# Kernel tuning notes

Measured on AMD Instinct MI355X. Metric: run time of the kernel, lower is better.

Reference implementation:

```python
import jax, jax.numpy as jnp
import numpy as np

N = 100_000   # nodes in batched graph
E = 1_000_000 # edges
B = 1024      # graphs in batch
H = 64        # hidden_dim


def setup_inputs() -> dict:
    key = jax.random.key(0)
    ks = jax.random.split(key, 12)
    u_flag = jax.random.randint(ks[0], (N,), 0, 2) > 0
    v_flag = jax.random.randint(ks[1], (N,), 0, 2) > 0
    src = jax.random.randint(ks[2], (E,), 0, N, dtype=jnp.int32)
    dst = jax.random.randint(ks[3], (E,), 0, N, dtype=jnp.int32)
    # contiguous graph assignment so every graph is non-empty
    node2graph = ((jnp.arange(N, dtype=jnp.int32) * B) // N).astype(jnp.int32)
    s = 0.05
    params = {
        'W0': jax.random.normal(ks[4], (2, H), jnp.float32) * s,
        'b0': jnp.zeros((H,), jnp.float32),
        'eps0': jnp.zeros((), jnp.float32),
        'W1': jax.random.normal(ks[5], (H, H), jnp.float32) * s,
        'b1': jnp.zeros((H,), jnp.float32),
        'eps1': jnp.zeros((), jnp.float32),
        'W2': jax.random.normal(ks[6], (H, H), jnp.float32) * s,
        'b2': jnp.zeros((H,), jnp.float32),
        'eps2': jnp.zeros((), jnp.float32),
        'Ws1': jax.random.normal(ks[7], (H, H), jnp.float32) * s,
        'bs1': jnp.zeros((H,), jnp.float32),
        'Ws2': jax.random.normal(ks[8], (H, 1), jnp.float32) * s,
        'bs2': jnp.zeros((1,), jnp.float32),
    }
    return dict(u_flag=u_flag, v_flag=v_flag, src=src, dst=dst,
                node2graph=node2graph, **params)


def _gin_layer(h, src, dst, W, b, eps):
    # GINConv: MLP((1+eps)*h + sum_{j->i} h_j), apply_func = Linear
    agg = jax.ops.segment_sum(h[src], dst, num_segments=N)  # [N,H_in]
    z = (1.0 + eps) * h + agg
    return jax.nn.relu(z @ W + b)


def reference(u_flag, v_flag, src, dst, node2graph,
              W0, b0, eps0, W1, b1, eps1, W2, b2, eps2,
              Ws1, bs1, Ws2, bs2):
    # one-hot node features from u/v masks: feat[:,0]=u, feat[:,1]=v
    feat = jnp.stack([u_flag, v_flag], axis=-1).astype(jnp.float32)  # [N,2]
    h = _gin_layer(feat, src, dst, W0, b0, eps0)
    h = _gin_layer(h, src, dst, W1, b1, eps1)
    h = _gin_layer(h, src, dst, W2, b2, eps2)  # [N,H]
    # per-graph mean pooling (dgl.mean_nodes)
    sums = jax.ops.segment_sum(h, node2graph, num_segments=B)          # [B,H]
    cnts = jax.ops.segment_sum(jnp.ones((N,), jnp.float32), node2graph,
                               num_segments=B)                         # [B]
    hg = sums / jnp.maximum(cnts, 1.0)[:, None]
    # Scorer: Linear -> ReLU -> Linear -> sigmoid
    z = jax.nn.relu(hg @ Ws1 + bs1)
    return jax.nn.sigmoid(z @ Ws2 + bs2)[:, 0]  # (B,)
```

## Files before the change

### kernel.cpp

```cpp
#include <hip/hip_runtime.h>
#include <hip/hip_bf16.h>
#include <math.h>

#define NN 100000
#define NE 1000000
#define NB 1024
#define NCHUNK 6250
#define NRNG 256
#define RANGE 391
#define NBK 512
#define EPB 1954

typedef __attribute__((ext_vector_type(8))) short short8v;
typedef __attribute__((ext_vector_type(4))) float f32x4;

union frag16 { uint4 u; short8v s; };

static __device__ __forceinline__ float bf_lo(unsigned int u) {
    return __uint_as_float(u << 16);
}
static __device__ __forceinline__ float bf_hi(unsigned int u) {
    return __uint_as_float(u & 0xffff0000u);
}
static __device__ __forceinline__ unsigned int bf16_rne(float f) {
    unsigned int u = __float_as_uint(f);
    return (u + 0x7fffu + ((u >> 16) & 1u)) >> 16;
}
static __device__ __forceinline__ unsigned int pack_bf16(float a, float b) {
    return bf16_rne(a) | (bf16_rne(b) << 16);
}

__global__ __launch_bounds__(256) void featb_kernel(
        const void* __restrict__ u, const void* __restrict__ v,
        unsigned char* __restrict__ featb,
        const int* __restrict__ n2g, int* __restrict__ gstart, int n) {
    __shared__ int flag_s;
    const int tid = threadIdx.x;
    int c = 0;
    {
        const unsigned char* p = (const unsigned char*)u + tid * 4;
        c = (p[0] != 0) + (p[1] != 0) + (p[2] != 0) + (p[3] != 0);
    }
    #pragma unroll
    for (int off = 32; off > 0; off >>= 1) c += __shfl_xor(c, off);
    if (tid == 0) flag_s = 0;
    __syncthreads();
    if ((tid & 63) == 0) atomicAdd(&flag_s, c);
    __syncthreads();
    bool is_u8 = (4 * flag_s > 1024);
    int i = blockIdx.x * blockDim.x + tid;
    if (i >= n) return;
    unsigned char fu, fv;
    if (is_u8) {
        fu = ((const unsigned char*)u)[i] ? 1 : 0;
        fv = ((const unsigned char*)v)[i] ? 1 : 0;
    } else {
        fu = ((const int*)u)[i] ? 1 : 0;
        fv = ((const int*)v)[i] ? 1 : 0;
    }
    featb[i] = fu | (fv << 1);
    int g = n2g[i];
    if (i == 0) {
        gstart[g] = 0;
        gstart[NB] = n;
    } else if (n2g[i - 1] != g) {
        gstart[g] = i;
    }
}

__global__ __launch_bounds__(256) void bcount_kernel(const int* __restrict__ dst,
                                                     int* __restrict__ bcnt, int e) {
    __shared__ int hc[NRNG];
    hc[threadIdx.x] = 0;
    __syncthreads();
    const int blk = blockIdx.x, lo = blk * EPB, hi = min(e, lo + EPB);
    for (int i = lo + threadIdx.x; i < hi; i += 256)
        atomicAdd(&hc[dst[i] / RANGE], 1);
    __syncthreads();
    bcnt[threadIdx.x * NBK + blk] = hc[threadIdx.x];
}

__global__ __launch_bounds__(256) void bsum_kernel(const int* __restrict__ bcnt,
                                                   int* __restrict__ btot) {
    __shared__ int s[4];
    const int b = blockIdx.x, tid = threadIdx.x;
    int c = bcnt[b * NBK + tid] + bcnt[b * NBK + 256 + tid];
    #pragma unroll
    for (int off = 32; off > 0; off >>= 1) c += __shfl_xor(c, off);
    if ((tid & 63) == 0) s[tid >> 6] = c;
    __syncthreads();
    if (tid == 0) btot[b] = s[0] + s[1] + s[2] + s[3];
}

__global__ __launch_bounds__(256) void bbase_kernel(const int* __restrict__ bcnt,
                                                    const int* __restrict__ btot,
                                                    int* __restrict__ bstart,
                                                    int* __restrict__ bbase) {
    __shared__ int s[256];
    const int b = blockIdx.x, tid = threadIdx.x;
    int v = btot[tid];
    s[tid] = v;
    __syncthreads();
    for (int off = 1; off < 256; off <<= 1) {
        int t = (tid >= off) ? s[tid - off] : 0;
        __syncthreads();
        s[tid] += t;
        __syncthreads();
    }
    if (b == 0) {
        bstart[tid] = s[tid] - v;
        if (tid == 255) bstart[NRNG] = s[tid];
    }
    const int exb = s[b] - btot[b];
    __syncthreads();
    int2 c = ((const int2*)(bcnt + b * NBK))[tid];
    int lsum = c.x + c.y;
    s[tid] = lsum;
    __syncthreads();
    for (int off = 1; off < 256; off <<= 1) {
        int t = (tid >= off) ? s[tid - off] : 0;
        __syncthreads();
        s[tid] += t;
        __syncthreads();
    }
    int run = exb + s[tid] - lsum;
    ((int2*)(bbase + b * NBK))[tid] = make_int2(run, run + c.x);
}

__global__ __launch_bounds__(256) void bwrite_kernel(const int* __restrict__ src,
                                                     const int* __restrict__ dst,
                                                     const int* __restrict__ bbase,
                                                     unsigned int* __restrict__ ebuck, int e) {
    __shared__ int cur[NRNG];
    const int blk = blockIdx.x;
    cur[threadIdx.x] = bbase[threadIdx.x * NBK + blk];
    __syncthreads();
    const int lo = blk * EPB, hi = min(e, lo + EPB);
    for (int i = lo + threadIdx.x; i < hi; i += 256) {
        int d = dst[i];
        int b = d / RANGE;
        int dloc = d - b * RANGE;
        int pos = atomicAdd(&cur[b], 1);
        ebuck[pos] = (unsigned int)src[i] | ((unsigned int)dloc << 17);
    }
}

__global__ __launch_bounds__(256) void build_kernel(
        const unsigned int* __restrict__ ebuck, const int* __restrict__ bstart,
        const unsigned char* __restrict__ featb,
        const float* __restrict__ W0, const float* __restrict__ b0,
        const float* __restrict__ epsp,
        int* __restrict__ rowptr, int* __restrict__ esrc,
        unsigned short* __restrict__ hout) {
    __shared__ unsigned long long hloc[RANGE];
    __shared__ int cur[RANGE];
    __shared__ int sscan[256];
    __shared__ float w0s[128];
    __shared__ float b0s[64];
    const int r = blockIdx.x, tid = threadIdx.x;
    const int nlo = r * RANGE;
    const int nr = min(NN, nlo + RANGE) - nlo;
    for (int i = tid; i < nr; i += 256) hloc[i] = 0ull;
    if (tid < 128) w0s[tid] = W0[tid];
    if (tid >= 128 && tid < 192) b0s[tid - 128] = b0[tid - 128];
    __syncthreads();
    const int elo = bstart[r], ehi = bstart[r + 1];
    for (int i = elo + tid; i < ehi; i += 256) {
        unsigned int u = ebuck[i];
        unsigned char f = featb[u & 0x1FFFFu];
        unsigned long long inc = 1ull
            | ((unsigned long long)(f & 1) << 21)
            | ((unsigned long long)(f >> 1) << 42);
        atomicAdd(&hloc[u >> 17], inc);
    }
    __syncthreads();
    const int base = tid * 2;
    int ldeg[2];
    int lsum = 0;
    #pragma unroll
    for (int j = 0; j < 2; ++j) {
        int i = base + j;
        ldeg[j] = (i < nr) ? (int)(hloc[i] & 0x1FFFFFull) : 0;
        lsum += ldeg[j];
    }
    sscan[tid] = lsum;
    __syncthreads();
    for (int off = 1; off < 256; off <<= 1) {
        int t = (tid >= off) ? sscan[tid - off] : 0;
        __syncthreads();
        sscan[tid] += t;
        __syncthreads();
    }
    int run = elo + sscan[tid] - lsum;
    #pragma unroll
    for (int j = 0; j < 2; ++j) {
        int i = base + j;
        if (i < nr) {
            rowptr[nlo + i] = run;
            cur[i] = run;
            run += ldeg[j];
        }
    }
    if (r == NRNG - 1 && tid == 0) rowptr[NN] = bstart[NRNG];
    __syncthreads();
    for (int i = elo + tid; i < ehi; i += 256) {
        unsigned int u = ebuck[i];
        int pos = atomicAdd(&cur[u >> 17], 1);
        esrc[pos] = (int)(u & 0x1FFFFu);
    }
    const float e = 1.0f + epsp[0];
    for (int idx = tid; idx < nr * 8; idx += 256) {
        int i = idx >> 3, oct = idx & 7;
        unsigned long long hv = hloc[i];
        float cu = (float)((hv >> 21) & 0x1FFFFFull);
        float cv = (float)(hv >> 42);
        unsigned char f = featb[nlo + i];
        float z0 = fmaf(e, (float)(f & 1), cu);
        float z1 = fmaf(e, (float)(f >> 1), cv);
        unsigned int p[4];
        #pragma unroll
        for (int k = 0; k < 4; ++k) {
            int c0 = oct * 8 + 2 * k;
            float o0 = fmaxf(fmaf(z0, w0s[c0],     fmaf(z1, w0s[64 + c0],     b0s[c0])),     0.0f);
            float o1 = fmaxf(fmaf(z0, w0s[c0 + 1], fmaf(z1, w0s[64 + c0 + 1], b0s[c0 + 1])), 0.0f);
            p[k] = pack_bf16(o0, o1);
        }
        ((uint4*)(hout + (size_t)(nlo + i) * 64))[oct] = make_uint4(p[0], p[1], p[2], p[3]);
    }
}

__global__ __launch_bounds__(64) void wprep_kernel(const float* __restrict__ W1,
                                                   const float* __restrict__ W2,
                                                   uint4* __restrict__ wpk1,
                                                   uint4* __restrict__ wpk2) {
    const float* W = blockIdx.x ? W2 : W1;
    uint4* wpk = blockIdx.x ? wpk2 : wpk1;
    const int lane = threadIdx.x;
    const int bcol = lane & 15;
    const int krow = (lane >> 4) * 8;
    #pragma unroll
    for (int n = 0; n < 4; ++n) {
        #pragma unroll
        for (int t = 0; t < 2; ++t) {
            unsigned int p[4];
            #pragma unroll
            for (int jj = 0; jj < 4; ++jj) {
                int k0 = t * 32 + krow + 2 * jj;
                float w0 = W[(size_t)k0 * 64 + n * 16 + bcol];
                float w1 = W[(size_t)(k0 + 1) * 64 + n * 16 + bcol];
                p[jj] = pack_bf16(w0, w1);
            }
            wpk[(n * 2 + t) * 64 + lane] = make_uint4(p[0], p[1], p[2], p[3]);
        }
    }
}

__global__ __launch_bounds__(256) void gin_layer_kernel(
        const int* __restrict__ rowptr, const int* __restrict__ esrc,
        const unsigned short* __restrict__ hin,
        const uint4* __restrict__ wpk, const float* __restrict__ b,
        const float* __restrict__ epsp, unsigned short* __restrict__ hout) {
    __shared__ __align__(16) unsigned char zall[4][2048];
    const int tid = threadIdx.x;
    const int lane = tid & 63;
    const int g = lane >> 3;
    const int sub = lane & 7;
    unsigned char* zw = &zall[tid >> 6][0];
    const float ep = 1.0f + epsp[0];

    const int bcol = (lane & 15);
    frag16 Bf[4][2];
    #pragma unroll
    for (int n = 0; n < 4; ++n) {
        #pragma unroll
        for (int t = 0; t < 2; ++t)
            Bf[n][t].u = wpk[(n * 2 + t) * 64 + lane];
    }
    float bj[4];
    #pragma unroll
    for (int n = 0; n < 4; ++n) bj[n] = b[n * 16 + bcol];

    const int wid = (blockIdx.x * blockDim.x + tid) >> 6;
    const int nwaves = (gridDim.x * blockDim.x) >> 6;

    for (int chunk = wid; chunk < NCHUNK; chunk += nwaves) {
        const int cbase_n = chunk * 16;
        #pragma unroll
        for (int b8 = 0; b8 < 2; ++b8) {
            int node = cbase_n + b8 * 8 + g;
            int e0 = rowptr[node], e1 = rowptr[node + 1];
            int deg = e1 - e0;
            uint4 ov = ((const uint4*)(hin + (size_t)node * 64))[sub];
            float acc[8];
            #pragma unroll
            for (int c = 0; c < 8; ++c) acc[c] = 0.0f;
            int md = deg;
            md = max(md, __shfl_xor(md, 8));
            md = max(md, __shfl_xor(md, 16));
            md = max(md, __shfl_xor(md, 32));
            #pragma unroll 4
            for (int t = 0; t < md; ++t) {
                int em = max(min(e0 + t, e1 - 1), 0);
                int sraw = esrc[em];
                bool act = (t < deg);
                int s = act ? sraw : node;
                uint4 v = ((const uint4*)(hin + (size_t)s * 64))[sub];
                float m = act ? 1.0f : 0.0f;
                acc[0] = fmaf(m, bf_lo(v.x), acc[0]);
                acc[1] = fmaf(m, bf_hi(v.x), acc[1]);
                acc[2] = fmaf(m, bf_lo(v.y), acc[2]);
                acc[3] = fmaf(m, bf_hi(v.y), acc[3]);
                acc[4] = fmaf(m, bf_lo(v.z), acc[4]);
                acc[5] = fmaf(m, bf_hi(v.z), acc[5]);
                acc[6] = fmaf(m, bf_lo(v.w), acc[6]);
                acc[7] = fmaf(m, bf_hi(v.w), acc[7]);
            }
            acc[0] = fmaf(ep, bf_lo(ov.x), acc[0]);
            acc[1] = fmaf(ep, bf_hi(ov.x), acc[1]);
            acc[2] = fmaf(ep, bf_lo(ov.y), acc[2]);
            acc[3] = fmaf(ep, bf_hi(ov.y), acc[3]);
            acc[4] = fmaf(ep, bf_lo(ov.z), acc[4]);
            acc[5] = fmaf(ep, bf_hi(ov.z), acc[5]);
            acc[6] = fmaf(ep, bf_lo(ov.w), acc[6]);
            acc[7] = fmaf(ep, bf_hi(ov.w), acc[7]);
            uint4 pk = make_uint4(pack_bf16(acc[0], acc[1]), pack_bf16(acc[2], acc[3]),
                                  pack_bf16(acc[4], acc[5]), pack_bf16(acc[6], acc[7]));
            int row = b8 * 8 + g;
            *(uint4*)&zw[row * 128 + ((sub ^ g) << 4)] = pk;
        }
        const int arow = lane & 15;
        const int hi = lane >> 4;
        frag16 a0, a1;
        a0.u = *(const uint4*)&zw[arow * 128 + (((hi + 0) ^ (lane & 7)) << 4)];
        a1.u = *(const uint4*)&zw[arow * 128 + (((hi + 4) ^ (lane & 7)) << 4)];
        #pragma unroll
        for (int n = 0; n < 4; ++n) {
            f32x4 c = {bj[n], bj[n], bj[n], bj[n]};
            c = __builtin_amdgcn_mfma_f32_16x16x32_bf16(a0.s, Bf[n][0].s, c, 0, 0, 0);
            c = __builtin_amdgcn_mfma_f32_16x16x32_bf16(a1.s, Bf[n][1].s, c, 0, 0, 0);
            #pragma unroll
            for (int q = 0; q < 4; ++q) {
                int rr = hi * 4 + q;
                float v = fmaxf(c[q], 0.0f);
                hout[(size_t)(cbase_n + rr) * 64 + n * 16 + bcol] =
                    (unsigned short)bf16_rne(v);
            }
        }
    }
}

__global__ __launch_bounds__(256) void pool_scorer_kernel(
        const unsigned short* __restrict__ h, const int* __restrict__ gstart,
        const float* __restrict__ Ws1, const float* __restrict__ bs1,
        const float* __restrict__ Ws2, const float* __restrict__ bs2,
        float* __restrict__ out) {
    int g = blockIdx.x * 4 + (threadIdx.x >> 6);
    int lane = threadIdx.x & 63;
    if (g >= NB) return;
    int s0 = gstart[g], s1 = gstart[g + 1];
    float a0 = 0.0f, a1 = 0.0f, a2 = 0.0f, a3 = 0.0f;
    int i = s0;
    for (; i + 4 <= s1; i += 4) {
        a0 += __uint_as_float((unsigned int)h[(size_t)(i    ) * 64 + lane] << 16);
        a1 += __uint_as_float((unsigned int)h[(size_t)(i + 1) * 64 + lane] << 16);
        a2 += __uint_as_float((unsigned int)h[(size_t)(i + 2) * 64 + lane] << 16);
        a3 += __uint_as_float((unsigned int)h[(size_t)(i + 3) * 64 + lane] << 16);
    }
    for (; i < s1; ++i)
        a0 += __uint_as_float((unsigned int)h[(size_t)i * 64 + lane] << 16);
    float mean = ((a0 + a1) + (a2 + a3)) / fmaxf((float)(s1 - s0), 1.0f);
    float o = bs1[lane];
    #pragma unroll 8
    for (int k = 0; k < 64; ++k)
        o = fmaf(__shfl(mean, k), Ws1[(size_t)k * 64 + lane], o);
    float z = fmaxf(o, 0.0f) * Ws2[lane];
    #pragma unroll
    for (int off = 32; off > 0; off >>= 1) z += __shfl_xor(z, off);
    if (lane == 0) out[g] = 1.0f / (1.0f + expf(-(z + bs2[0])));
}

extern "C" void kernel_launch(void* const* d_in, const int* in_sizes, int n_in,
                              void* d_out, int out_size, void* d_ws, size_t ws_size,
                              hipStream_t stream) {
    const void*  u_flag = d_in[0];
    const void*  v_flag = d_in[1];
    const int*   src    = (const int*)d_in[2];
    const int*   dst    = (const int*)d_in[3];
    const int*   n2g    = (const int*)d_in[4];
    const float* W0     = (const float*)d_in[5];
    const float* b0     = (const float*)d_in[6];
    const float* eps0   = (const float*)d_in[7];
    const float* W1     = (const float*)d_in[8];
    const float* b1     = (const float*)d_in[9];
    const float* eps1   = (const float*)d_in[10];
    const float* W2     = (const float*)d_in[11];
    const float* b2     = (const float*)d_in[12];
    const float* eps2   = (const float*)d_in[13];
    const float* Ws1    = (const float*)d_in[14];
    const float* bs1    = (const float*)d_in[15];
    const float* Ws2    = (const float*)d_in[16];
    const float* bs2    = (const float*)d_in[17];
    float* out = (float*)d_out;

    int*    ws     = (int*)d_ws;
    int*    rowptr = ws;
    int*    gstart = ws + 100008;
    unsigned char* featb = (unsigned char*)(ws + 101036);
    unsigned short* h_a = (unsigned short*)(ws + 126036);
    unsigned short* h_b = (unsigned short*)(ws + 3326036);
    int*    esrc   = ws + 6526036;
    int*    bcnt   = ws + 7526036;
    int*    bbase  = ws + 7657108;
    int*    bstart = ws + 7788180;
    int*    btot   = ws + 7788440;
    unsigned int* ebuck = (unsigned int*)(ws + 7788696);
    uint4*  wpk1   = (uint4*)(ws + 8788696);
    uint4*  wpk2   = (uint4*)(ws + 8790744);

    const int B256 = 256;

    featb_kernel<<<(NN + B256 - 1) / B256, B256, 0, stream>>>(u_flag, v_flag, featb,
                                                              n2g, gstart, NN);

    wprep_kernel<<<2, 64, 0, stream>>>(W1, W2, wpk1, wpk2);

    bcount_kernel<<<NBK, B256, 0, stream>>>(dst, bcnt, NE);
    bsum_kernel<<<NRNG, B256, 0, stream>>>(bcnt, btot);
    bbase_kernel<<<NRNG, B256, 0, stream>>>(bcnt, btot, bstart, bbase);
    bwrite_kernel<<<NBK, B256, 0, stream>>>(src, dst, bbase, ebuck, NE);

    build_kernel<<<NRNG, B256, 0, stream>>>(ebuck, bstart, featb, W0, b0, eps0,
                                            rowptr, esrc, h_a);

    gin_layer_kernel<<<1563, 256, 0, stream>>>(rowptr, esrc, h_a, wpk1, b1, eps1, h_b);
    gin_layer_kernel<<<1563, 256, 0, stream>>>(rowptr, esrc, h_b, wpk2, b2, eps2, h_a);

    pool_scorer_kernel<<<NB / 4, 256, 0, stream>>>(h_a, gstart, Ws1, bs1, Ws2, bs2, out);
}
```

Measured before the change: 137.6 us.

## Merge prep kernels into fewer launches and batch edge-index loads via shuffles

The featb and bcount kernels are merged into one launch using a block-index split, and the bsum and wprep kernels are merged the same way, which removes two kernel launches and their gaps. In the GIN aggregation loop, each 8-lane group now loads eight source indices at once, one per lane, and broadcasts them with shuffles. Before, every lane loaded the same index on every iteration. This cuts redundant index loads and the serial dependency on them, at the cost of extra shuffle instructions.

```diff
diff --git a/kernel.cpp b/kernel.cpp
--- a/kernel.cpp
+++ b/kernel.cpp
@@ -10,6 +10,7 @@
 #define RANGE 391
 #define NBK 512
 #define EPB 1954
+#define FEATB_BLKS 392
 
 typedef __attribute__((ext_vector_type(8))) short short8v;
 typedef __attribute__((ext_vector_type(4))) float f32x4;
@@ -30,66 +31,93 @@
     return bf16_rne(a) | (bf16_rne(b) << 16);
 }
 
-__global__ __launch_bounds__(256) void featb_kernel(
+__global__ __launch_bounds__(256) void prep_kernel(
         const void* __restrict__ u, const void* __restrict__ v,
         unsigned char* __restrict__ featb,
-        const int* __restrict__ n2g, int* __restrict__ gstart, int n) {
-    __shared__ int flag_s;
+        const int* __restrict__ n2g, int* __restrict__ gstart,
+        const int* __restrict__ dst, int* __restrict__ bcnt) {
+    __shared__ int sh[NRNG];
     const int tid = threadIdx.x;
-    int c = 0;
-    {
-        const unsigned char* p = (const unsigned char*)u + tid * 4;
-        c = (p[0] != 0) + (p[1] != 0) + (p[2] != 0) + (p[3] != 0);
-    }
-    #pragma unroll
-    for (int off = 32; off > 0; off >>= 1) c += __shfl_xor(c, off);
-    if (tid == 0) flag_s = 0;
-    __syncthreads();
-    if ((tid & 63) == 0) atomicAdd(&flag_s, c);
-    __syncthreads();
-    bool is_u8 = (4 * flag_s > 1024);
-    int i = blockIdx.x * blockDim.x + tid;
-    if (i >= n) return;
-    unsigned char fu, fv;
-    if (is_u8) {
-        fu = ((const unsigned char*)u)[i] ? 1 : 0;
-        fv = ((const unsigned char*)v)[i] ? 1 : 0;
+    if (blockIdx.x < FEATB_BLKS) {
+        int c;
+        {
+            const unsigned char* p = (const unsigned char*)u + tid * 4;
+            c = (p[0] != 0) + (p[1] != 0) + (p[2] != 0) + (p[3] != 0);
+        }
+        #pragma unroll
+        for (int off = 32; off > 0; off >>= 1) c += __shfl_xor(c, off);
+        if (tid == 0) sh[0] = 0;
+        __syncthreads();
+        if ((tid & 63) == 0) atomicAdd(&sh[0], c);
+        __syncthreads();
+        bool is_u8 = (4 * sh[0] > 1024);
+        int i = blockIdx.x * 256 + tid;
+        if (i >= NN) return;
+        unsigned char fu, fv;
+        if (is_u8) {
+            fu = ((const unsigned char*)u)[i] ? 1 : 0;
+            fv = ((const unsigned char*)v)[i] ? 1 : 0;
+        } else {
+            fu = ((const int*)u)[i] ? 1 : 0;
+            fv = ((const int*)v)[i] ? 1 : 0;
+        }
+        featb[i] = fu | (fv << 1);
+        int g = n2g[i];
+        if (i == 0) {
+            gstart[g] = 0;
+            gstart[NB] = NN;
+        } else if (n2g[i - 1] != g) {
+            gstart[g] = i;
+        }
     } else {
-        fu = ((const int*)u)[i] ? 1 : 0;
-        fv = ((const int*)v)[i] ? 1 : 0;
-    }
-    featb[i] = fu | (fv << 1);
-    int g = n2g[i];
-    if (i == 0) {
-        gstart[g] = 0;
-        gstart[NB] = n;
-    } else if (n2g[i - 1] != g) {
-        gstart[g] = i;
-    }
-}
-
-__global__ __launch_bounds__(256) void bcount_kernel(const int* __restrict__ dst,
-                                                     int* __restrict__ bcnt, int e) {
-    __shared__ int hc[NRNG];
-    hc[threadIdx.x] = 0;
-    __syncthreads();
-    const int blk = blockIdx.x, lo = blk * EPB, hi = min(e, lo + EPB);
-    for (int i = lo + threadIdx.x; i < hi; i += 256)
-        atomicAdd(&hc[dst[i] / RANGE], 1);
-    __syncthreads();
-    bcnt[threadIdx.x * NBK + blk] = hc[threadIdx.x];
-}
-
-__global__ __launch_bounds__(256) void bsum_kernel(const int* __restrict__ bcnt,
-                                                   int* __restrict__ btot) {
+        const int blk = blockIdx.x - FEATB_BLKS;
+        sh[tid] = 0;
+        __syncthreads();
+        const int lo = blk * EPB, hi = min(NE, lo + EPB);
+        for (int i = lo + tid; i < hi; i += 256)
+            atomicAdd(&sh[dst[i] / RANGE], 1);
+        __syncthreads();
+        bcnt[tid * NBK + blk] = sh[tid];
+    }
+}
+
+__global__ __launch_bounds__(256) void wsum_kernel(
+        const int* __restrict__ bcnt, int* __restrict__ btot,
+        const float* __restrict__ W1, const float* __restrict__ W2,
+        uint4* __restrict__ wpk1, uint4* __restrict__ wpk2) {
     __shared__ int s[4];
-    const int b = blockIdx.x, tid = threadIdx.x;
-    int c = bcnt[b * NBK + tid] + bcnt[b * NBK + 256 + tid];
-    #pragma unroll
-    for (int off = 32; off > 0; off >>= 1) c += __shfl_xor(c, off);
-    if ((tid & 63) == 0) s[tid >> 6] = c;
-    __syncthreads();
-    if (tid == 0) btot[b] = s[0] + s[1] + s[2] + s[3];
+    const int tid = threadIdx.x;
+    if (blockIdx.x < NRNG) {
+        const int b = blockIdx.x;
+        int c = bcnt[b * NBK + tid] + bcnt[b * NBK + 256 + tid];
+        #pragma unroll
+        for (int off = 32; off > 0; off >>= 1) c += __shfl_xor(c, off);
+        if ((tid & 63) == 0) s[tid >> 6] = c;
+        __syncthreads();
+        if (tid == 0) btot[b] = s[0] + s[1] + s[2] + s[3];
+    } else {
+        if (tid >= 64) return;
+        const float* W = (blockIdx.x == NRNG) ? W1 : W2;
+        uint4* wpk = (blockIdx.x == NRNG) ? wpk1 : wpk2;
+        const int lane = tid;
+        const int bcol = lane & 15;
+        const int krow = (lane >> 4) * 8;
+        #pragma unroll
+        for (int n = 0; n < 4; ++n) {
+            #pragma unroll
+            for (int t = 0; t < 2; ++t) {
+                unsigned int p[4];
+                #pragma unroll
+                for (int jj = 0; jj < 4; ++jj) {
+                    int k0 = t * 32 + krow + 2 * jj;
+                    float w0 = W[(size_t)k0 * 64 + n * 16 + bcol];
+                    float w1 = W[(size_t)(k0 + 1) * 64 + n * 16 + bcol];
+                    p[jj] = pack_bf16(w0, w1);
+                }
+                wpk[(n * 2 + t) * 64 + lane] = make_uint4(p[0], p[1], p[2], p[3]);
+            }
+        }
+    }
 }
 
 __global__ __launch_bounds__(256) void bbase_kernel(const int* __restrict__ bcnt,
@@ -229,32 +257,6 @@
     }
 }
 
-__global__ __launch_bounds__(64) void wprep_kernel(const float* __restrict__ W1,
-                                                   const float* __restrict__ W2,
-                                                   uint4* __restrict__ wpk1,
-                                                   uint4* __restrict__ wpk2) {
-    const float* W = blockIdx.x ? W2 : W1;
-    uint4* wpk = blockIdx.x ? wpk2 : wpk1;
-    const int lane = threadIdx.x;
-    const int bcol = lane & 15;
-    const int krow = (lane >> 4) * 8;
-    #pragma unroll
-    for (int n = 0; n < 4; ++n) {
-        #pragma unroll
-        for (int t = 0; t < 2; ++t) {
-            unsigned int p[4];
-            #pragma unroll
-            for (int jj = 0; jj < 4; ++jj) {
-                int k0 = t * 32 + krow + 2 * jj;
-                float w0 = W[(size_t)k0 * 64 + n * 16 + bcol];
-                float w1 = W[(size_t)(k0 + 1) * 64 + n * 16 + bcol];
-                p[jj] = pack_bf16(w0, w1);
-            }
-            wpk[(n * 2 + t) * 64 + lane] = make_uint4(p[0], p[1], p[2], p[3]);
-        }
-    }
-}
-
 __global__ __launch_bounds__(256) void gin_layer_kernel(
         const int* __restrict__ rowptr, const int* __restrict__ esrc,
         const unsigned short* __restrict__ hin,
@@ -298,22 +300,26 @@
             md = max(md, __shfl_xor(md, 8));
             md = max(md, __shfl_xor(md, 16));
             md = max(md, __shfl_xor(md, 32));
-            #pragma unroll 4
-            for (int t = 0; t < md; ++t) {
-                int em = max(min(e0 + t, e1 - 1), 0);
-                int sraw = esrc[em];
-                bool act = (t < deg);
-                int s = act ? sraw : node;
-                uint4 v = ((const uint4*)(hin + (size_t)s * 64))[sub];
-                float m = act ? 1.0f : 0.0f;
-                acc[0] = fmaf(m, bf_lo(v.x), acc[0]);
-                acc[1] = fmaf(m, bf_hi(v.x), acc[1]);
-                acc[2] = fmaf(m, bf_lo(v.y), acc[2]);
-                acc[3] = fmaf(m, bf_hi(v.y), acc[3]);
-                acc[4] = fmaf(m, bf_lo(v.z), acc[4]);
-                acc[5] = fmaf(m, bf_hi(v.z), acc[5]);
-                acc[6] = fmaf(m, bf_lo(v.w), acc[6]);
-                acc[7] = fmaf(m, bf_hi(v.w), acc[7]);
+            for (int tb = 0; tb < md; tb += 8) {
+                int ei = max(min(e0 + tb + sub, e1 - 1), 0);
+                int sidx = esrc[ei];
+                #pragma unroll 4
+                for (int tt = 0; tt < 8; ++tt) {
+                    int t = tb + tt;
+                    int s_ = __shfl(sidx, (lane & 56) + tt);
+                    bool act = (t < deg);
+                    int s = act ? s_ : node;
+                    uint4 v = ((const uint4*)(hin + (size_t)s * 64))[sub];
+                    float m = act ? 1.0f : 0.0f;
+                    acc[0] = fmaf(m, bf_lo(v.x), acc[0]);
+                    acc[1] = fmaf(m, bf_hi(v.x), acc[1]);
+                    acc[2] = fmaf(m, bf_lo(v.y), acc[2]);
+                    acc[3] = fmaf(m, bf_hi(v.y), acc[3]);
+                    acc[4] = fmaf(m, bf_lo(v.z), acc[4]);
+                    acc[5] = fmaf(m, bf_hi(v.z), acc[5]);
+                    acc[6] = fmaf(m, bf_lo(v.w), acc[6]);
+                    acc[7] = fmaf(m, bf_hi(v.w), acc[7]);
+                }
             }
             acc[0] = fmaf(ep, bf_lo(ov.x), acc[0]);
             acc[1] = fmaf(ep, bf_hi(ov.x), acc[1]);
@@ -419,13 +425,11 @@
 
     const int B256 = 256;
 
-    featb_kernel<<<(NN + B256 - 1) / B256, B256, 0, stream>>>(u_flag, v_flag, featb,
-                                                              n2g, gstart, NN);
-
-    wprep_kernel<<<2, 64, 0, stream>>>(W1, W2, wpk1, wpk2);
-
-    bcount_kernel<<<NBK, B256, 0, stream>>>(dst, bcnt, NE);
-    bsum_kernel<<<NRNG, B256, 0, stream>>>(bcnt, btot);
+    prep_kernel<<<FEATB_BLKS + NBK, B256, 0, stream>>>(u_flag, v_flag, featb,
+                                                       n2g, gstart, dst, bcnt);
+
+    wsum_kernel<<<NRNG + 2, B256, 0, stream>>>(bcnt, btot, W1, W2, wpk1, wpk2);
+
     bbase_kernel<<<NRNG, B256, 0, stream>>>(bcnt, btot, bstart, bbase);
     bwrite_kernel<<<NBK, B256, 0, stream>>>(src, dst, bbase, ebuck, NE);
 
```

New measurement: 146.1 us. 1.06x slower.
